# Kernel tuning notes

Measured on AMD Instinct MI355X. Metric: run time of the kernel, lower is better.

Reference implementation:

```python
import jax, jax.numpy as jnp
import numpy as np

N = 50000
E = 800000
C_IN, C_HID, C_OUT = 128, 64, 1


def setup_inputs() -> dict:
    key = jax.random.key(0)
    ks = jax.random.split(key, 8)
    x = jax.random.normal(ks[0], (N, C_IN), dtype=jnp.float32)
    edge_index = jax.random.randint(ks[1], (2, E), 0, N, dtype=jnp.int64)
    # GCNConv linear params (glorot-ish scaling)
    W1 = jax.random.normal(ks[2], (C_IN, C_HID), dtype=jnp.float32) / np.sqrt(C_IN)
    b1 = jnp.zeros((C_HID,), dtype=jnp.float32)
    W2 = jax.random.normal(ks[3], (C_HID, C_HID), dtype=jnp.float32) / np.sqrt(C_HID)
    b2 = jnp.zeros((C_HID,), dtype=jnp.float32)
    W3 = jax.random.normal(ks[4], (C_HID, C_OUT), dtype=jnp.float32) / np.sqrt(C_HID)
    b3 = jnp.zeros((C_OUT,), dtype=jnp.float32)
    return {"x": x, "edge_index": edge_index, "W1": W1, "b1": b1,
            "W2": W2, "b2": b2, "W3": W3, "b3": b3}


def _gcn_norm(edge_index, num_nodes):
    # Add self-loops, compute symmetric normalization D^{-1/2} A D^{-1/2}
    loop = jnp.arange(num_nodes, dtype=edge_index.dtype)
    src = jnp.concatenate([edge_index[0], loop])  # message sources
    dst = jnp.concatenate([edge_index[1], loop])  # message targets
    ones = jnp.ones(src.shape[0], dtype=jnp.float32)
    deg = jax.ops.segment_sum(ones, dst, num_segments=num_nodes)
    dis = jnp.where(deg > 0, jax.lax.rsqrt(jnp.maximum(deg, 1.0)), 0.0)
    norm = dis[src] * dis[dst]  # [E+N]
    return src, dst, norm


def _gcn_conv(h, src, dst, norm, W, b, num_nodes):
    h = h @ W                                  # [N, C_out]
    msg = h[src] * norm[:, None]               # gather + scale, [E+N, C_out]
    out = jax.ops.segment_sum(msg, dst, num_segments=num_nodes)  # scatter-add
    return out + b


def reference(x, edge_index, W1, b1, W2, b2, W3, b3):
    num_nodes = x.shape[0]
    src, dst, norm = _gcn_norm(edge_index, num_nodes)
    leaky = lambda v: jnp.where(v >= 0, v, 0.01 * v)
    h = _gcn_conv(x, src, dst, norm, W1, b1, num_nodes)
    h = leaky(h)
    h = _gcn_conv(h, src, dst, norm, W2, b2, num_nodes)
    h = leaky(h)
    h = _gcn_conv(h, src, dst, norm, W3, b3, num_nodes)
    return h
```

## Files before the change

### kernel.cpp

```cpp
#include <hip/hip_runtime.h>

#define CIN 128
#define CHID 64
#define CSTRIDE 64

__device__ __forceinline__ float leaky(float v) { return v >= 0.f ? v : 0.01f * v; }
__device__ __forceinline__ float bcast(float v, int k) {
    return __int_as_float(__builtin_amdgcn_readlane(__float_as_int(v), k));
}
__device__ __forceinline__ void acc4(float4& a, const float4 v) {
    a.x += v.x; a.y += v.y; a.z += v.z; a.w += v.w;
}

__global__ void k_deg(const int* __restrict__ dst, const int* __restrict__ src,
                      int* __restrict__ deg, unsigned short* __restrict__ csr, int E) {
    int e = blockIdx.x * 256 + threadIdx.x;
    if (e >= E) return;
    int d = dst[e];
    int slot = atomicAdd(&deg[d], 1);
    if (slot < CSTRIDE) csr[(d << 6) + slot] = (unsigned short)src[e];
}

__global__ __launch_bounds__(256) void k_gemm1(
    const float* __restrict__ x, const float* __restrict__ W,
    const int* __restrict__ deg, float* __restrict__ hp, int N) {
    const int wave = threadIdx.x >> 6, lane = threadIdx.x & 63;
    float w[CIN];
#pragma unroll
    for (int k = 0; k < CIN; ++k) w[k] = W[k * CHID + lane];
    const int stride = gridDim.x * 4;
    for (int n = blockIdx.x * 4 + wave; n < N; n += stride) {
        float x0 = x[(size_t)n * CIN + lane];
        float x1 = x[(size_t)n * CIN + 64 + lane];
        float acc0 = 0.f, acc1 = 0.f;
#pragma unroll
        for (int k = 0; k < 64; k += 2) {
            acc0 = fmaf(bcast(x0, k),     w[k],     acc0);
            acc1 = fmaf(bcast(x0, k + 1), w[k + 1], acc1);
        }
#pragma unroll
        for (int k = 0; k < 64; k += 2) {
            acc0 = fmaf(bcast(x1, k),     w[64 + k],     acc0);
            acc1 = fmaf(bcast(x1, k + 1), w[64 + k + 1], acc1);
        }
        float dn = rsqrtf((float)(deg[n] + 1));
        hp[(size_t)n * CHID + lane] = dn * (acc0 + acc1);
    }
}

__global__ __launch_bounds__(256) void kG1(
    const unsigned short* __restrict__ csr, const int* __restrict__ deg,
    const float* __restrict__ hp, const float* __restrict__ W2,
    const float* __restrict__ b1, float* __restrict__ hp2, int N) {
    const int wave = threadIdx.x >> 6, lane = threadIdx.x & 63;
    const int g = lane >> 4, sl = lane & 15;
    float w[CHID];
#pragma unroll
    for (int k = 0; k < CHID; ++k) w[k] = W2[k * CHID + lane];
    const float4 bb = ((const float4*)b1)[sl];
    const float4* __restrict__ hpq = (const float4*)hp;
    const int stride = gridDim.x * 4;
    for (int n = blockIdx.x * 4 + wave; n < N; n += stride) {
        int d = deg[n], base = n << 6;
        float4 a0 = make_float4(0.f, 0.f, 0.f, 0.f), a1 = a0, a2 = a0, a3 = a0;
        if (g == 0) a0 = hpq[(size_t)n * 16 + sl];
        for (int b = g; b < d; b += 16) {
            { int s = csr[base + b];      acc4(a0, hpq[(size_t)s * 16 + sl]); }
            if (b + 4 < d)  { int s = csr[base + b + 4];  acc4(a1, hpq[(size_t)s * 16 + sl]); }
            if (b + 8 < d)  { int s = csr[base + b + 8];  acc4(a2, hpq[(size_t)s * 16 + sl]); }
            if (b + 12 < d) { int s = csr[base + b + 12]; acc4(a3, hpq[(size_t)s * 16 + sl]); }
        }
        acc4(a0, a1); acc4(a2, a3); acc4(a0, a2);
        a0.x += __shfl_xor(a0.x, 16, 64); a0.y += __shfl_xor(a0.y, 16, 64);
        a0.z += __shfl_xor(a0.z, 16, 64); a0.w += __shfl_xor(a0.w, 16, 64);
        a0.x += __shfl_xor(a0.x, 32, 64); a0.y += __shfl_xor(a0.y, 32, 64);
        a0.z += __shfl_xor(a0.z, 32, 64); a0.w += __shfl_xor(a0.w, 32, 64);
        float dn = rsqrtf((float)(d + 1));
        float4 gv;
        gv.x = leaky(dn * a0.x + bb.x);
        gv.y = leaky(dn * a0.y + bb.y);
        gv.z = leaky(dn * a0.z + bb.z);
        gv.w = leaky(dn * a0.w + bb.w);
        float acc0 = 0.f, acc1 = 0.f;
#pragma unroll
        for (int i = 0; i < 16; ++i) {
            acc0 = fmaf(bcast(gv.x, i), w[4 * i + 0], acc0);
            acc1 = fmaf(bcast(gv.y, i), w[4 * i + 1], acc1);
            acc0 = fmaf(bcast(gv.z, i), w[4 * i + 2], acc0);
            acc1 = fmaf(bcast(gv.w, i), w[4 * i + 3], acc1);
        }
        hp2[(size_t)n * CHID + lane] = dn * (acc0 + acc1);
    }
}

__global__ __launch_bounds__(256) void kG2(
    const unsigned short* __restrict__ csr, const int* __restrict__ deg,
    const float* __restrict__ hp, const float* __restrict__ b2,
    const float* __restrict__ W3, float* __restrict__ hp3, int N) {
    const int wave = threadIdx.x >> 6, lane = threadIdx.x & 63;
    const int g = lane >> 4, sl = lane & 15;
    const float4 bb = ((const float4*)b2)[sl];
    const float4 w3 = ((const float4*)W3)[sl];
    const float4* __restrict__ hpq = (const float4*)hp;
    const int stride = gridDim.x * 4;
    for (int n = blockIdx.x * 4 + wave; n < N; n += stride) {
        int d = deg[n], base = n << 6;
        float4 a0 = make_float4(0.f, 0.f, 0.f, 0.f), a1 = a0, a2 = a0, a3 = a0;
        if (g == 0) a0 = hpq[(size_t)n * 16 + sl];
        for (int b = g; b < d; b += 16) {
            { int s = csr[base + b];      acc4(a0, hpq[(size_t)s * 16 + sl]); }
            if (b + 4 < d)  { int s = csr[base + b + 4];  acc4(a1, hpq[(size_t)s * 16 + sl]); }
            if (b + 8 < d)  { int s = csr[base + b + 8];  acc4(a2, hpq[(size_t)s * 16 + sl]); }
            if (b + 12 < d) { int s = csr[base + b + 12]; acc4(a3, hpq[(size_t)s * 16 + sl]); }
        }
        acc4(a0, a1); acc4(a2, a3); acc4(a0, a2);
        a0.x += __shfl_xor(a0.x, 16, 64); a0.y += __shfl_xor(a0.y, 16, 64);
        a0.z += __shfl_xor(a0.z, 16, 64); a0.w += __shfl_xor(a0.w, 16, 64);
        a0.x += __shfl_xor(a0.x, 32, 64); a0.y += __shfl_xor(a0.y, 32, 64);
        a0.z += __shfl_xor(a0.z, 32, 64); a0.w += __shfl_xor(a0.w, 32, 64);
        float dn = rsqrtf((float)(d + 1));
        float t = leaky(dn * a0.x + bb.x) * w3.x
                + leaky(dn * a0.y + bb.y) * w3.y
                + leaky(dn * a0.z + bb.z) * w3.z
                + leaky(dn * a0.w + bb.w) * w3.w;
        t += __shfl_xor(t, 1, 64); t += __shfl_xor(t, 2, 64);
        t += __shfl_xor(t, 4, 64); t += __shfl_xor(t, 8, 64);
        if (lane == 0) hp3[n] = dn * t;
    }
}

__global__ void kG3(const unsigned short* __restrict__ csr, const int* __restrict__ deg,
                    const float* __restrict__ hp3, const float* __restrict__ b3,
                    float* __restrict__ out, int N) {
    int t = blockIdx.x * 256 + threadIdx.x;
    int node = t >> 4, sl = t & 15;
    if (node >= N) return;
    int d = deg[node], base = node << 6;
    float acc = (sl == 0) ? hp3[node] : 0.f;
    for (int i = sl; i < d; i += 16) acc += hp3[(int)csr[base + i]];
#pragma unroll
    for (int off = 8; off > 0; off >>= 1) acc += __shfl_down(acc, off, 16);
    if (sl == 0) out[node] = rsqrtf((float)(d + 1)) * acc + b3[0];
}

extern "C" void kernel_launch(void* const* d_in, const int* in_sizes, int n_in,
                              void* d_out, int out_size, void* d_ws, size_t ws_size,
                              hipStream_t stream) {
    const float* x  = (const float*)d_in[0];
    const int*   ei = (const int*)d_in[1];
    const float* W1 = (const float*)d_in[2];
    const float* b1 = (const float*)d_in[3];
    const float* W2 = (const float*)d_in[4];
    const float* b2 = (const float*)d_in[5];
    const float* W3 = (const float*)d_in[6];
    const float* b3 = (const float*)d_in[7];

    const int N = in_sizes[0] / CIN;
    const int E = in_sizes[1] / 2;
    const int* src = ei;
    const int* dst = ei + E;

    char* w = (char*)d_ws;
    auto take = [&](size_t bytes) { char* p = w; w += (bytes + 255) & ~(size_t)255; return p; };
    int*            deg = (int*)take((size_t)N * 4);
    unsigned short* csr = (unsigned short*)take((size_t)N * CSTRIDE * 2);
    float*          A   = (float*)take((size_t)N * CHID * 4);
    float*          B   = (float*)take((size_t)N * CHID * 4);
    float*          hp3 = (float*)take((size_t)N * 4);

    hipMemsetAsync(deg, 0, (size_t)N * 4, stream);

    k_deg  <<<(E + 255) / 256, 256, 0, stream>>>(dst, src, deg, csr, E);
    k_gemm1<<<1024, 256, 0, stream>>>(x, W1, deg, A, N);
    kG1    <<<2048, 256, 0, stream>>>(csr, deg, A, W2, b1, B, N);
    kG2    <<<2048, 256, 0, stream>>>(csr, deg, B, b2, W3, hp3, N);
    kG3    <<<(N * 16 + 255) / 256, 256, 0, stream>>>(csr, deg, hp3, b3, (float*)d_out, N);
}
```

Before: 234.0 us.

## Shard CSR build by destination range and gather four nodes per wave

The degree/CSR build kernel now has each block handle one of eight destination-node shards. Every shard re-reads the full edge list, but its atomics stay within a narrower address range, which is meant to improve atomic locality across XCDs. The aggregation kernels now map one node to each 16-lane group, so a wave covers four nodes instead of one. They read the neighbour list as packed 32-bit pairs with unrolled loads to expose more memory-level parallelism. kG1 also moves W2 into shared memory instead of holding 64 registers, computes its matmul with shuffles plus float4 LDS reads, and writes float4 outputs. In exchange it reads the edge list eight times over and spends extra LDS traffic per node.

```diff
diff --git a/kernel.cpp b/kernel.cpp
--- a/kernel.cpp
+++ b/kernel.cpp
@@ -13,12 +13,21 @@
 }
 
 __global__ void k_deg(const int* __restrict__ dst, const int* __restrict__ src,
-                      int* __restrict__ deg, unsigned short* __restrict__ csr, int E) {
-    int e = blockIdx.x * 256 + threadIdx.x;
-    if (e >= E) return;
-    int d = dst[e];
-    int slot = atomicAdd(&deg[d], 1);
-    if (slot < CSTRIDE) csr[(d << 6) + slot] = (unsigned short)src[e];
+                      int* __restrict__ deg, unsigned short* __restrict__ csr,
+                      int E, int nps, int N) {
+    const int shard = blockIdx.x & 7;
+    const int chunk = blockIdx.x >> 3;
+    const int nchunks = gridDim.x >> 3;
+    const int lo = shard * nps;
+    const int hi = min(lo + nps, N);
+    const int estride = nchunks * 256;
+    for (int e = chunk * 256 + threadIdx.x; e < E; e += estride) {
+        int d = dst[e];
+        if (d >= lo && d < hi) {
+            int slot = atomicAdd(&deg[d], 1);
+            if (slot < CSTRIDE) csr[(d << 6) + slot] = (unsigned short)src[e];
+        }
+    }
 }
 
 __global__ __launch_bounds__(256) void k_gemm1(
@@ -48,48 +57,89 @@
     }
 }
 
+#define GATHER_GROUP(hpq, csr32, deg, nb)                                        \
+    const int n = (nb) + g;                                                      \
+    const bool ok = (n < N);                                                     \
+    const int d = ok ? deg[n] : 0;                                               \
+    const int base32 = n << 5;                                                   \
+    unsigned int c[8];                                                           \
+_Pragma("unroll")                                                                \
+    for (int k = 0; k < 8; ++k) c[k] = ok ? csr32[base32 + k] : 0u;              \
+    float4 A0 = make_float4(0.f, 0.f, 0.f, 0.f), A1 = A0, A2 = A0, A3 = A0;      \
+    if (ok) A0 = hpq[(size_t)n * 16 + sl];                   \
+_Pragma("unroll")                                                                \
+    for (int k = 0; k < 8; ++k) {                                                \
+        int s0 = (int)(c[k] & 0xffffu), s1 = (int)(c[k] >> 16);                  \
+        if ((k & 1) == 0) {                                                      \
+            if (2 * k     < d) acc4(A0, hpq[(size_t)s0 * 16 + sl]);              \
+            if (2 * k + 1 < d) acc4(A1, hpq[(size_t)s1 * 16 + sl]);              \
+        } else {                                                                 \
+            if (2 * k     < d) acc4(A2, hpq[(size_t)s0 * 16 + sl]);              \
+            if (2 * k + 1 < d) acc4(A3, hpq[(size_t)s1 * 16 + sl]);              \
+        }                                                                        \
+    }                                                                            \
+    for (int b = 16; b < d; b += 16) {                                           \
+        unsigned int ct[8];                                                      \
+_Pragma("unroll")                                                                \
+        for (int k = 0; k < 8; ++k) ct[k] = csr32[base32 + (b >> 1) + k];        \
+_Pragma("unroll")                                                                \
+        for (int k = 0; k < 8; ++k) {                                            \
+            int s0 = (int)(ct[k] & 0xffffu), s1 = (int)(ct[k] >> 16);            \
+            if ((k & 1) == 0) {                                                  \
+                if (b + 2 * k     < d) acc4(A0, hpq[(size_t)s0 * 16 + sl]);      \
+                if (b + 2 * k + 1 < d) acc4(A1, hpq[(size_t)s1 * 16 + sl]);      \
+            } else {                                                             \
+                if (b + 2 * k     < d) acc4(A2, hpq[(size_t)s0 * 16 + sl]);      \
+                if (b + 2 * k + 1 < d) acc4(A3, hpq[(size_t)s1 * 16 + sl]);      \
+            }                                                                    \
+        }                                                                        \
+    }                                                                            \
+    acc4(A0, A1); acc4(A2, A3); acc4(A0, A2);
+
 __global__ __launch_bounds__(256) void kG1(
     const unsigned short* __restrict__ csr, const int* __restrict__ deg,
     const float* __restrict__ hp, const float* __restrict__ W2,
     const float* __restrict__ b1, float* __restrict__ hp2, int N) {
+    __shared__ float W2s[CHID * CHID];
+    for (int i = threadIdx.x; i < CHID * CHID; i += 256) W2s[i] = W2[i];
+    __syncthreads();
     const int wave = threadIdx.x >> 6, lane = threadIdx.x & 63;
-    const int g = lane >> 4, sl = lane & 15;
-    float w[CHID];
-#pragma unroll
-    for (int k = 0; k < CHID; ++k) w[k] = W2[k * CHID + lane];
+    const int g = lane >> 4, sl = lane & 15, lbase = lane & 48;
     const float4 bb = ((const float4*)b1)[sl];
     const float4* __restrict__ hpq = (const float4*)hp;
-    const int stride = gridDim.x * 4;
-    for (int n = blockIdx.x * 4 + wave; n < N; n += stride) {
-        int d = deg[n], base = n << 6;
-        float4 a0 = make_float4(0.f, 0.f, 0.f, 0.f), a1 = a0, a2 = a0, a3 = a0;
-        if (g == 0) a0 = hpq[(size_t)n * 16 + sl];
-        for (int b = g; b < d; b += 16) {
-            { int s = csr[base + b];      acc4(a0, hpq[(size_t)s * 16 + sl]); }
-            if (b + 4 < d)  { int s = csr[base + b + 4];  acc4(a1, hpq[(size_t)s * 16 + sl]); }
-            if (b + 8 < d)  { int s = csr[base + b + 8];  acc4(a2, hpq[(size_t)s * 16 + sl]); }
-            if (b + 12 < d) { int s = csr[base + b + 12]; acc4(a3, hpq[(size_t)s * 16 + sl]); }
-        }
-        acc4(a0, a1); acc4(a2, a3); acc4(a0, a2);
-        a0.x += __shfl_xor(a0.x, 16, 64); a0.y += __shfl_xor(a0.y, 16, 64);
-        a0.z += __shfl_xor(a0.z, 16, 64); a0.w += __shfl_xor(a0.w, 16, 64);
-        a0.x += __shfl_xor(a0.x, 32, 64); a0.y += __shfl_xor(a0.y, 32, 64);
-        a0.z += __shfl_xor(a0.z, 32, 64); a0.w += __shfl_xor(a0.w, 32, 64);
+    const unsigned int* __restrict__ csr32 = (const unsigned int*)csr;
+    const float4* __restrict__ W2q = (const float4*)W2s;
+    const int stride = gridDim.x * 16;
+    for (int nb = blockIdx.x * 16 + wave * 4; nb < N; nb += stride) {
+        GATHER_GROUP(hpq, csr32, deg, nb)
         float dn = rsqrtf((float)(d + 1));
         float4 gv;
-        gv.x = leaky(dn * a0.x + bb.x);
-        gv.y = leaky(dn * a0.y + bb.y);
-        gv.z = leaky(dn * a0.z + bb.z);
-        gv.w = leaky(dn * a0.w + bb.w);
-        float acc0 = 0.f, acc1 = 0.f;
+        gv.x = leaky(dn * A0.x + bb.x);
+        gv.y = leaky(dn * A0.y + bb.y);
+        gv.z = leaky(dn * A0.z + bb.z);
+        gv.w = leaky(dn * A0.w + bb.w);
+        float4 o = make_float4(0.f, 0.f, 0.f, 0.f);
 #pragma unroll
         for (int i = 0; i < 16; ++i) {
-            acc0 = fmaf(bcast(gv.x, i), w[4 * i + 0], acc0);
-            acc1 = fmaf(bcast(gv.y, i), w[4 * i + 1], acc1);
-            acc0 = fmaf(bcast(gv.z, i), w[4 * i + 2], acc0);
-            acc1 = fmaf(bcast(gv.w, i), w[4 * i + 3], acc1);
-        }
-        hp2[(size_t)n * CHID + lane] = dn * (acc0 + acc1);
+            float gx = __shfl(gv.x, lbase + i, 64);
+            float gy = __shfl(gv.y, lbase + i, 64);
+            float gz = __shfl(gv.z, lbase + i, 64);
+            float gw = __shfl(gv.w, lbase + i, 64);
+            float4 w0 = W2q[(4 * i + 0) * 16 + sl];
+            float4 w1 = W2q[(4 * i + 1) * 16 + sl];
+            float4 w2 = W2q[(4 * i + 2) * 16 + sl];
+            float4 w3v = W2q[(4 * i + 3) * 16 + sl];
+            o.x = fmaf(gx, w0.x, o.x); o.y = fmaf(gx, w0.y, o.y);
+            o.z = fmaf(gx, w0.z, o.z); o.w = fmaf(gx, w0.w, o.w);
+            o.x = fmaf(gy, w1.x, o.x); o.y = fmaf(gy, w1.y, o.y);
+            o.z = fmaf(gy, w1.z, o.z); o.w = fmaf(gy, w1.w, o.w);
+            o.x = fmaf(gz, w2.x, o.x); o.y = fmaf(gz, w2.y, o.y);
+            o.z = fmaf(gz, w2.z, o.z); o.w = fmaf(gz, w2.w, o.w);
+            o.x = fmaf(gw, w3v.x, o.x); o.y = fmaf(gw, w3v.y, o.y);
+            o.z = fmaf(gw, w3v.z, o.z); o.w = fmaf(gw, w3v.w, o.w);
+        }
+        if (ok) ((float4*)hp2)[(size_t)n * 16 + sl] =
+            make_float4(dn * o.x, dn * o.y, dn * o.z, dn * o.w);
     }
 }
 
@@ -102,30 +152,18 @@
     const float4 bb = ((const float4*)b2)[sl];
     const float4 w3 = ((const float4*)W3)[sl];
     const float4* __restrict__ hpq = (const float4*)hp;
-    const int stride = gridDim.x * 4;
-    for (int n = blockIdx.x * 4 + wave; n < N; n += stride) {
-        int d = deg[n], base = n << 6;
-        float4 a0 = make_float4(0.f, 0.f, 0.f, 0.f), a1 = a0, a2 = a0, a3 = a0;
-        if (g == 0) a0 = hpq[(size_t)n * 16 + sl];
-        for (int b = g; b < d; b += 16) {
-            { int s = csr[base + b];      acc4(a0, hpq[(size_t)s * 16 + sl]); }
-            if (b + 4 < d)  { int s = csr[base + b + 4];  acc4(a1, hpq[(size_t)s * 16 + sl]); }
-            if (b + 8 < d)  { int s = csr[base + b + 8];  acc4(a2, hpq[(size_t)s * 16 + sl]); }
-            if (b + 12 < d) { int s = csr[base + b + 12]; acc4(a3, hpq[(size_t)s * 16 + sl]); }
-        }
-        acc4(a0, a1); acc4(a2, a3); acc4(a0, a2);
-        a0.x += __shfl_xor(a0.x, 16, 64); a0.y += __shfl_xor(a0.y, 16, 64);
-        a0.z += __shfl_xor(a0.z, 16, 64); a0.w += __shfl_xor(a0.w, 16, 64);
-        a0.x += __shfl_xor(a0.x, 32, 64); a0.y += __shfl_xor(a0.y, 32, 64);
-        a0.z += __shfl_xor(a0.z, 32, 64); a0.w += __shfl_xor(a0.w, 32, 64);
+    const unsigned int* __restrict__ csr32 = (const unsigned int*)csr;
+    const int stride = gridDim.x * 16;
+    for (int nb = blockIdx.x * 16 + wave * 4; nb < N; nb += stride) {
+        GATHER_GROUP(hpq, csr32, deg, nb)
         float dn = rsqrtf((float)(d + 1));
-        float t = leaky(dn * a0.x + bb.x) * w3.x
-                + leaky(dn * a0.y + bb.y) * w3.y
-                + leaky(dn * a0.z + bb.z) * w3.z
-                + leaky(dn * a0.w + bb.w) * w3.w;
+        float t = leaky(dn * A0.x + bb.x) * w3.x
+                + leaky(dn * A0.y + bb.y) * w3.y
+                + leaky(dn * A0.z + bb.z) * w3.z
+                + leaky(dn * A0.w + bb.w) * w3.w;
         t += __shfl_xor(t, 1, 64); t += __shfl_xor(t, 2, 64);
         t += __shfl_xor(t, 4, 64); t += __shfl_xor(t, 8, 64);
-        if (lane == 0) hp3[n] = dn * t;
+        if (ok && sl == 0) hp3[n] = dn * t;
     }
 }
 
@@ -159,6 +197,7 @@
     const int E = in_sizes[1] / 2;
     const int* src = ei;
     const int* dst = ei + E;
+    const int nps = (N + 7) / 8;
 
     char* w = (char*)d_ws;
     auto take = [&](size_t bytes) { char* p = w; w += (bytes + 255) & ~(size_t)255; return p; };
@@ -170,7 +209,7 @@
 
     hipMemsetAsync(deg, 0, (size_t)N * 4, stream);
 
-    k_deg  <<<(E + 255) / 256, 256, 0, stream>>>(dst, src, deg, csr, E);
+    k_deg  <<<2048, 256, 0, stream>>>(dst, src, deg, csr, E, nps, N);
     k_gemm1<<<1024, 256, 0, stream>>>(x, W1, deg, A, N);
     kG1    <<<2048, 256, 0, stream>>>(csr, deg, A, W2, b1, B, N);
     kG2    <<<2048, 256, 0, stream>>>(csr, deg, B, b2, W3, hp3, N);
```

Result: no change. 234.1 us (+0.0%).
